# Kernel optimization log

Measured on AMD Instinct MI355X. Metric: run time of the kernel, lower is better.

## Reference

```python
import jax, jax.numpy as jnp
import numpy as np
from jax import lax

C = 768
CLS = 20
HEADS = 4
EPS = 1e-5


def setup_inputs() -> dict:
    key = jax.random.key(0)
    ks = jax.random.split(key, 16)
    B, Hp, Wp = 16, 32, 32
    s = 0.02
    return {
        "x_cls": jax.random.normal(ks[0], (B, CLS, C), jnp.float32),
        "input_patch": jax.random.normal(ks[1], (B, C, Hp, Wp), jnp.float32),
        # norm_cls (nn.LayerNorm)
        "ln_cls_w": jnp.ones((C,), jnp.float32),
        "ln_cls_b": jnp.zeros((C,), jnp.float32),
        # norm_x (LayerNormGeneral, affine_shape=(C,1,1))
        "nx_w": jnp.ones((C, 1, 1), jnp.float32),
        "nx_b": jnp.zeros((C, 1, 1), jnp.float32),
        # proj_q: Linear(C, C)
        "Wq": jax.random.normal(ks[2], (C, C), jnp.float32) * s,
        "bq": jnp.zeros((C,), jnp.float32),
        # proj_kv: Conv2d(C, 2C, 1)
        "Wkv": jax.random.normal(ks[3], (2 * C, C), jnp.float32) * s,
        "bkv": jnp.zeros((2 * C,), jnp.float32),
        # proj: Linear(C, C)
        "Wp": jax.random.normal(ks[4], (C, C), jnp.float32) * s,
        "bp": jnp.zeros((C,), jnp.float32),
        # proj_patch: Conv2d(CLS, C, 3, 1, 1) + BatchNorm2d(C) (eval) + GELU
        "Wconv": jax.random.normal(ks[5], (C, CLS, 3, 3), jnp.float32) * s,
        "bconv": jnp.zeros((C,), jnp.float32),
        "bn_g": jnp.ones((C,), jnp.float32),
        "bn_b": jnp.zeros((C,), jnp.float32),
        "bn_m": jnp.zeros((C,), jnp.float32),
        "bn_v": jnp.ones((C,), jnp.float32),
    }


def _layernorm_last(x, w, b):
    mu = x.mean(-1, keepdims=True)
    var = ((x - mu) ** 2).mean(-1, keepdims=True)
    return (x - mu) / jnp.sqrt(var + EPS) * w + b


def _layernorm_general(x, w, b):
    # normalized_dim=(1,2,3) on [B,C,H,W]; affine shape (C,1,1)
    mu = x.mean((1, 2, 3), keepdims=True)
    c = x - mu
    s = (c ** 2).mean((1, 2, 3), keepdims=True)
    return c / jnp.sqrt(s + EPS) * w + b


def reference(x_cls, input_patch, ln_cls_w, ln_cls_b, nx_w, nx_b, Wq, bq,
              Wkv, bkv, Wp, bp, Wconv, bconv, bn_g, bn_b, bn_m, bn_v):
    B, Cls, Cc = x_cls.shape
    Hp, Wpx = input_patch.shape[2:]
    dh = Cc // HEADS
    scale = dh ** (-0.5)

    # Q from cls tokens
    q = _layernorm_last(x_cls, ln_cls_w, ln_cls_b) @ Wq.T + bq  # [B,Cls,C]
    q = q.reshape(B, Cls, HEADS, dh).transpose(0, 2, 1, 3)      # [B,H,Cls,dh]

    # KV from conv patch features
    nx = _layernorm_general(input_patch, nx_w, nx_b)            # [B,C,Hp,Wp]
    kv = jnp.einsum('bchw,oc->bohw', nx, Wkv) + bkv[:, None, None]  # [B,2C,Hp,Wp]
    k, v = kv[:, :Cc], kv[:, Cc:]
    key = k.reshape(B, HEADS, dh, Hp * Wpx)                     # [B,H,dh,N]
    val = v.reshape(B, HEADS, dh, Hp * Wpx).transpose(0, 1, 3, 2)  # [B,H,N,dh]

    attn = jax.nn.softmax(jnp.einsum('bhcd,bhdn->bhcn', q, key) * scale, axis=-1)
    out = jnp.einsum('bhcn,bhnd->bhcd', attn, val)              # [B,H,Cls,dh]
    out = out.transpose(0, 2, 1, 3).reshape(B, Cls, Cc)
    out_cls = x_cls + (out @ Wp.T + bp)                         # proj_drop is identity (p=0)

    # semantic-to-feature projection
    patch_flat = input_patch.reshape(B, Cc, Hp * Wpx)           # [B,C,N]
    out_patch = jnp.einsum('blc,bcn->bln', out_cls, patch_flat) # [B,Cls,N]
    out_patch = out_patch.reshape(B, Cls, Hp, Wpx)

    y = lax.conv_general_dilated(out_patch, Wconv, (1, 1), 'SAME',
                                 dimension_numbers=('NCHW', 'OIHW', 'NCHW'))
    y = y + bconv[:, None, None]
    y = (y - bn_m[:, None, None]) / jnp.sqrt(bn_v[:, None, None] + EPS) \
        * bn_g[:, None, None] + bn_b[:, None, None]
    y = jax.nn.gelu(y, approximate=False)
    return out_cls, y
```

## Files before the change

kernel.cpp:

```cpp
#include <hip/hip_runtime.h>
#include <hip/hip_bf16.h>
#include <math.h>

typedef float f32x4 __attribute__((ext_vector_type(4)));
typedef __bf16 bf16x8 __attribute__((ext_vector_type(8)));
typedef __bf16 bf16x4 __attribute__((ext_vector_type(4)));


static constexpr size_t OFF_XT   = 0;
static constexpr size_t OFF_KT   = 25165824;
static constexpr size_t OFF_V    = 50331648;
static constexpr size_t OFF_WB   = 75497472;
static constexpr size_t OFF_RS   = 77856768;
static constexpr size_t OFF_CST  = 77862912;
static constexpr size_t OFF_PART = 77869056;
static constexpr size_t OFF_ST   = 77893632;
static constexpr size_t OFF_WQT  = 77893760;
static constexpr size_t OFF_WPT  = 80253056;
static constexpr size_t OFF_Q    = 82612352;
static constexpr size_t OFF_AO   = 83595392;
static constexpr size_t OFF_OP   = 84578432;

static constexpr size_t OFF_B2   = OFF_XT;
static constexpr size_t OFF_WCB  = OFF_XT + 6291456;
static constexpr size_t OFF_SC   = OFF_XT + 6586368;
static constexpr size_t OFF_SH   = OFF_XT + 6589440;

__global__ __launch_bounds__(256) void transpose_reduce(
    const float* __restrict__ x, __hip_bfloat16* __restrict__ xT,
    float* __restrict__ part) {
  __shared__ __hip_bfloat16 tile[64][66];
  __shared__ float red[4][2];
  int b = blockIdx.x, cb = blockIdx.y, nb = blockIdx.z;
  int t = threadIdx.x;
  const float* src = x + ((size_t)b * 768 + cb * 64) * 1024 + nb * 64;
  float s1 = 0.f, s2 = 0.f;
#pragma unroll
  for (int i = 0; i < 16; ++i) {
    int idx = i * 256 + t;
    int c = idx >> 6, n = idx & 63;
    float v = src[(size_t)c * 1024 + n];
    s1 += v; s2 += v * v;
    tile[c][n] = __float2bfloat16(v);
  }
#pragma unroll
  for (int o = 32; o > 0; o >>= 1) {
    s1 += __shfl_down(s1, o);
    s2 += __shfl_down(s2, o);
  }
  int wid = t >> 6, lane = t & 63;
  if (lane == 0) { red[wid][0] = s1; red[wid][1] = s2; }
  __syncthreads();
  if (t == 0) {
    float a = 0.f, bb = 0.f;
    for (int w = 0; w < 4; ++w) { a += red[w][0]; bb += red[w][1]; }
    int pidx = b * 192 + cb * 16 + nb;
    part[pidx * 2] = a; part[pidx * 2 + 1] = bb;
  }
  __hip_bfloat16* dst = xT + ((size_t)b * 1024 + nb * 64) * 768 + cb * 64;
#pragma unroll
  for (int i = 0; i < 16; ++i) {
    int idx = i * 256 + t;
    int n = idx >> 6, c = idx & 63;
    dst[(size_t)n * 768 + c] = tile[c][n];
  }
}

__global__ void finalize_stats(const float* __restrict__ part, float* __restrict__ st) {
  int t = threadIdx.x;
  if (t < 16) {
    float s1 = 0.f, s2 = 0.f;
    for (int i = 0; i < 192; ++i) {
      s1 += part[(t * 192 + i) * 2];
      s2 += part[(t * 192 + i) * 2 + 1];
    }
    float mu = s1 * (1.0f / 786432.0f);
    float var = s2 * (1.0f / 786432.0f) - mu * mu;
    st[t * 2] = mu;
    st[t * 2 + 1] = rsqrtf(var + 1e-5f);
  }
}

__global__ __launch_bounds__(256) void prep_wkv(
    const float* __restrict__ Wkv, const float* __restrict__ nxw,
    const float* __restrict__ nxb, const float* __restrict__ bkv,
    __hip_bfloat16* __restrict__ Wb, float* __restrict__ rowsum,
    float* __restrict__ cst) {
  int o = blockIdx.x * 4 + (threadIdx.x >> 6);
  int lane = threadIdx.x & 63;
  const float* wrow = Wkv + (size_t)o * 768;
  float rs = 0.f, cs = 0.f;
#pragma unroll
  for (int i = 0; i < 12; ++i) {
    int c = lane + i * 64;
    float w = wrow[c];
    float wb = w * nxw[c];
    Wb[(size_t)o * 768 + c] = __float2bfloat16(wb);
    rs += wb;
    cs += w * nxb[c];
  }
#pragma unroll
  for (int off = 32; off > 0; off >>= 1) {
    rs += __shfl_down(rs, off);
    cs += __shfl_down(cs, off);
  }
  if (lane == 0) { rowsum[o] = rs; cst[o] = cs + bkv[o]; }
}

__global__ __launch_bounds__(256) void transpose_w(
    const float* __restrict__ Wq, const float* __restrict__ Wp,
    float* __restrict__ WqT, float* __restrict__ WpT) {
  __shared__ float tl[64][65];
  const float* src = blockIdx.z ? Wp : Wq;
  float* dst = blockIdx.z ? WpT : WqT;
  int ot = blockIdx.x * 64, ct = blockIdx.y * 64;
  int t = threadIdx.x;
#pragma unroll
  for (int i = 0; i < 16; ++i) {
    int idx = i * 256 + t;
    int o = idx >> 6, c = idx & 63;
    tl[o][c] = src[(size_t)(ot + o) * 768 + ct + c];
  }
  __syncthreads();
#pragma unroll
  for (int i = 0; i < 16; ++i) {
    int idx = i * 256 + t;
    int c = idx >> 6, o = idx & 63;
    dst[(size_t)(ct + c) * 768 + ot + o] = tl[o][c];
  }
}

__global__ __launch_bounds__(256) void gemm_kv(
    const __hip_bfloat16* __restrict__ Wb, const __hip_bfloat16* __restrict__ xT,
    const float* __restrict__ rowsum, const float* __restrict__ cst,
    const float* __restrict__ st, __hip_bfloat16* __restrict__ KT,
    __hip_bfloat16* __restrict__ V) {
  __shared__ __hip_bfloat16 As[128 * 64];
  __shared__ __hip_bfloat16 Bs[128 * 64];
  int gx = blockIdx.x;
  int wg = (gx & 7) * 192 + (gx >> 3);
  int mt = wg % 12;
  int colt = wg / 12;
  int b = colt >> 3;
  int nt = colt & 7;
  int t = threadIdx.x;
  int wid = t >> 6, lane = t & 63;
  int wm = wid >> 1, wn = wid & 1;

  const __hip_bfloat16* Abase = Wb + (size_t)(mt * 128) * 768;
  const __hip_bfloat16* Bbase = xT + (size_t)b * 1024 * 768 + (size_t)(nt * 128) * 768;

  f32x4 acc[4][4] = {};

  for (int kt = 0; kt < 12; ++kt) {
    const __hip_bfloat16* ag = Abase + kt * 64;
    const __hip_bfloat16* bg = Bbase + kt * 64;
#pragma unroll
    for (int i = 0; i < 4; ++i) {
      int idx = i * 256 + t;
      int row = idx >> 3;
      int kc = (idx & 7) * 8;
      __builtin_amdgcn_global_load_lds(
          (const __attribute__((address_space(1))) void*)(ag + (size_t)row * 768 + kc),
          (__attribute__((address_space(3))) void*)(&As[idx * 8]), 16, 0, 0);
    }
#pragma unroll
    for (int i = 0; i < 4; ++i) {
      int idx = i * 256 + t;
      int row = idx >> 3;
      int kc = (idx & 7) * 8;
      __builtin_amdgcn_global_load_lds(
          (const __attribute__((address_space(1))) void*)(bg + (size_t)row * 768 + kc),
          (__attribute__((address_space(3))) void*)(&Bs[idx * 8]), 16, 0, 0);
    }
    __syncthreads();
#pragma unroll
    for (int kk = 0; kk < 2; ++kk) {
      bf16x8 af[4], bfv[4];
      int r = lane & 15, kc = kk * 32 + (lane >> 4) * 8;
#pragma unroll
      for (int mf = 0; mf < 4; ++mf)
        af[mf] = *(const bf16x8*)&As[(wm * 64 + mf * 16 + r) * 64 + kc];
#pragma unroll
      for (int nf = 0; nf < 4; ++nf)
        bfv[nf] = *(const bf16x8*)&Bs[(wn * 64 + nf * 16 + r) * 64 + kc];
#pragma unroll
      for (int mf = 0; mf < 4; ++mf)
#pragma unroll
        for (int nf = 0; nf < 4; ++nf)
          acc[mf][nf] = __builtin_amdgcn_mfma_f32_16x16x32_bf16(af[mf], bfv[nf], acc[mf][nf], 0, 0, 0);
    }
    __syncthreads();
  }
  float mu = st[b * 2], rstd = st[b * 2 + 1];
  if (mt < 6) {
    __hip_bfloat16* ktb = KT + (size_t)b * 1024 * 768;
#pragma unroll
    for (int mf = 0; mf < 4; ++mf) {
#pragma unroll
      for (int r = 0; r < 4; ++r) {
        int o = mt * 128 + wm * 64 + mf * 16 + (lane >> 4) * 4 + r;
        float corr = cst[o] - rstd * mu * rowsum[o];
#pragma unroll
        for (int nf = 0; nf < 4; ++nf) {
          int n = nt * 128 + wn * 64 + nf * 16 + (lane & 15);
          ktb[(size_t)n * 768 + o] = __float2bfloat16(rstd * acc[mf][nf][r] + corr);
        }
      }
    }
  } else {
    __hip_bfloat16* vb = V + (size_t)b * 768 * 1024;
#pragma unroll
    for (int mf = 0; mf < 4; ++mf) {
#pragma unroll
      for (int r = 0; r < 4; ++r) {
        int o = mt * 128 + wm * 64 + mf * 16 + (lane >> 4) * 4 + r;
        float corr = cst[o] - rstd * mu * rowsum[o];
        int ov = o - 768;
#pragma unroll
        for (int nf = 0; nf < 4; ++nf) {
          int n = nt * 128 + wn * 64 + nf * 16 + (lane & 15);
          vb[(size_t)ov * 1024 + n] = __float2bfloat16(rstd * acc[mf][nf][r] + corr);
        }
      }
    }
  }
}

__global__ __launch_bounds__(256) void q_proj(
    const float* __restrict__ x_cls, const float* __restrict__ lnw,
    const float* __restrict__ lnb, const float* __restrict__ WqT,
    const float* __restrict__ bq, __hip_bfloat16* __restrict__ Q) {
  __shared__ float xn[20 * 768];
  int b = blockIdx.x, ot = blockIdx.y;
  int t = threadIdx.x;
  const float* src = x_cls + (size_t)b * 20 * 768;
  for (int idx = t; idx < 15360; idx += 256) xn[idx] = src[idx];
  __syncthreads();
  int wid = t >> 6, lane = t & 63;
  for (int l = wid; l < 20; l += 4) {
    float s = 0.f;
#pragma unroll
    for (int i = 0; i < 12; ++i) s += xn[l * 768 + lane + i * 64];
#pragma unroll
    for (int o = 32; o > 0; o >>= 1) s += __shfl_down(s, o);
    s = __shfl(s, 0);
    float mu = s * (1.0f / 768.0f);
    float v = 0.f;
#pragma unroll
    for (int i = 0; i < 12; ++i) {
      float d = xn[l * 768 + lane + i * 64] - mu;
      v += d * d;
    }
#pragma unroll
    for (int o = 32; o > 0; o >>= 1) v += __shfl_down(v, o);
    v = __shfl(v, 0);
    float rstd = rsqrtf(v * (1.0f / 768.0f) + 1e-5f);
#pragma unroll
    for (int i = 0; i < 12; ++i) {
      int c = lane + i * 64;
      xn[l * 768 + c] = (xn[l * 768 + c] - mu) * rstd * lnw[c] + lnb[c];
    }
  }
  __syncthreads();
  int o = ot * 128 + (t & 127);
  int lg = t >> 7;
  float acc[10] = {};
  for (int c4 = 0; c4 < 768; c4 += 4) {
    float w0 = WqT[(size_t)(c4 + 0) * 768 + o];
    float w1 = WqT[(size_t)(c4 + 1) * 768 + o];
    float w2 = WqT[(size_t)(c4 + 2) * 768 + o];
    float w3 = WqT[(size_t)(c4 + 3) * 768 + o];
#pragma unroll
    for (int j = 0; j < 10; ++j) {
      const float4 a4 = *(const float4*)&xn[(lg * 10 + j) * 768 + c4];
      acc[j] += a4.x * w0 + a4.y * w1 + a4.z * w2 + a4.w * w3;
    }
  }
  float bqo = bq[o];
#pragma unroll
  for (int j = 0; j < 10; ++j)
    Q[((size_t)b * 20 + lg * 10 + j) * 768 + o] = __float2bfloat16(acc[j] + bqo);
}

__global__ __launch_bounds__(256) void attn_mfma(
    const __hip_bfloat16* __restrict__ Qbf, const __hip_bfloat16* __restrict__ KT,
    const __hip_bfloat16* __restrict__ V, float* __restrict__ AO) {
  __shared__ __hip_bfloat16 Qs[32 * 200];
  __shared__ __hip_bfloat16 Ps[32 * 1032];
  __shared__ float redm[4][32];
  __shared__ float reds[4][32];
  int b = blockIdx.x >> 2, h = blockIdx.x & 3;
  int t = threadIdx.x, w = t >> 6, lane = t & 63;
  int r16 = lane & 15, kg = lane >> 4;

  const __hip_bfloat16* qsrc = Qbf + (size_t)b * 20 * 768 + h * 192;
  for (int idx = t; idx < 32 * 192; idx += 256) {
    int l = idx / 192, d = idx % 192;
    Qs[l * 200 + d] = (l < 20) ? qsrc[(size_t)l * 768 + d] : __float2bfloat16(0.f);
  }
  __syncthreads();

  const __hip_bfloat16* ktb = KT + (size_t)b * 1024 * 768 + h * 192;
  int n0 = w * 256;
  f32x4 acc[2][16] = {};
  for (int ks = 0; ks < 6; ++ks) {
    bf16x8 af0 = *(const bf16x8*)&Qs[(r16) * 200 + ks * 32 + kg * 8];
    bf16x8 af1 = *(const bf16x8*)&Qs[(16 + r16) * 200 + ks * 32 + kg * 8];
#pragma unroll
    for (int nt = 0; nt < 16; ++nt) {
      bf16x8 bfv = *(const bf16x8*)&ktb[(size_t)(n0 + nt * 16 + r16) * 768 + ks * 32 + kg * 8];
      acc[0][nt] = __builtin_amdgcn_mfma_f32_16x16x32_bf16(af0, bfv, acc[0][nt], 0, 0, 0);
      acc[1][nt] = __builtin_amdgcn_mfma_f32_16x16x32_bf16(af1, bfv, acc[1][nt], 0, 0, 0);
    }
  }

#pragma unroll
  for (int mf = 0; mf < 2; ++mf) {
#pragma unroll
    for (int r = 0; r < 4; ++r) {
      float m = acc[mf][0][r];
#pragma unroll
      for (int nt = 1; nt < 16; ++nt) m = fmaxf(m, acc[mf][nt][r]);
#pragma unroll
      for (int o = 1; o < 16; o <<= 1) m = fmaxf(m, __shfl_xor(m, o));
      if (r16 == 0) redm[w][mf * 16 + kg * 4 + r] = m;
    }
  }
  __syncthreads();

  const float scale = 0.07216878364870322f;
#pragma unroll
  for (int mf = 0; mf < 2; ++mf) {
#pragma unroll
    for (int r = 0; r < 4; ++r) {
      int row = mf * 16 + kg * 4 + r;
      float M = fmaxf(fmaxf(redm[0][row], redm[1][row]),
                      fmaxf(redm[2][row], redm[3][row]));
      float s = 0.f;
#pragma unroll
      for (int nt = 0; nt < 16; ++nt) {
        float e = __expf((acc[mf][nt][r] - M) * scale);
        s += e;
        Ps[row * 1032 + n0 + nt * 16 + r16] = __float2bfloat16(e);
      }
#pragma unroll
      for (int o = 1; o < 16; o <<= 1) s += __shfl_xor(s, o);
      if (r16 == 0) reds[w][row] = s;
    }
  }
  __syncthreads();

  const __hip_bfloat16* vb = V + ((size_t)b * 768 + h * 192 + w * 48) * 1024;
  f32x4 pacc[2][3] = {};
  for (int ks = 0; ks < 32; ++ks) {
    bf16x8 pa0 = *(const bf16x8*)&Ps[(r16) * 1032 + ks * 32 + kg * 8];
    bf16x8 pa1 = *(const bf16x8*)&Ps[(16 + r16) * 1032 + ks * 32 + kg * 8];
#pragma unroll
    for (int nt = 0; nt < 3; ++nt) {
      bf16x8 vf = *(const bf16x8*)&vb[(size_t)(nt * 16 + r16) * 1024 + ks * 32 + kg * 8];
      pacc[0][nt] = __builtin_amdgcn_mfma_f32_16x16x32_bf16(pa0, vf, pacc[0][nt], 0, 0, 0);
      pacc[1][nt] = __builtin_amdgcn_mfma_f32_16x16x32_bf16(pa1, vf, pacc[1][nt], 0, 0, 0);
    }
  }

#pragma unroll
  for (int mf = 0; mf < 2; ++mf) {
#pragma unroll
    for (int r = 0; r < 4; ++r) {
      int row = mf * 16 + kg * 4 + r;
      if (row < 20) {
        float rinv = 1.0f / (reds[0][row] + reds[1][row] + reds[2][row] + reds[3][row]);
#pragma unroll
        for (int nt = 0; nt < 3; ++nt) {
          int d = w * 48 + nt * 16 + r16;
          AO[((size_t)b * 20 + row) * 768 + h * 192 + d] = pacc[mf][nt][r] * rinv;
        }
      }
    }
  }
}

__global__ __launch_bounds__(256) void cls_proj(
    const float* __restrict__ AO, const float* __restrict__ x_cls,
    const float* __restrict__ WpT, const float* __restrict__ bp,
    float* __restrict__ out_cls) {
  __shared__ float a[20 * 768];
  int b = blockIdx.x, ot = blockIdx.y;
  int t = threadIdx.x;
  const float* src = AO + (size_t)b * 15360;
  for (int idx = t; idx < 15360; idx += 256) a[idx] = src[idx];
  __syncthreads();
  int o = ot * 128 + (t & 127);
  int lg = t >> 7;
  float acc[10] = {};
  for (int c4 = 0; c4 < 768; c4 += 4) {
    float w0 = WpT[(size_t)(c4 + 0) * 768 + o];
    float w1 = WpT[(size_t)(c4 + 1) * 768 + o];
    float w2 = WpT[(size_t)(c4 + 2) * 768 + o];
    float w3 = WpT[(size_t)(c4 + 3) * 768 + o];
#pragma unroll
    for (int j = 0; j < 10; ++j) {
      const float4 a4 = *(const float4*)&a[(lg * 10 + j) * 768 + c4];
      acc[j] += a4.x * w0 + a4.y * w1 + a4.z * w2 + a4.w * w3;
    }
  }
  float bpo = bp[o];
#pragma unroll
  for (int j = 0; j < 10; ++j) {
    int l = lg * 10 + j;
    out_cls[((size_t)b * 20 + l) * 768 + o] =
        x_cls[((size_t)b * 20 + l) * 768 + o] + acc[j] + bpo;
  }
}

__global__ __launch_bounds__(256) void patch_mm(
    const float* __restrict__ out_cls, const float* __restrict__ x,
    float* __restrict__ OP) {
  __shared__ float a[20 * 768];
  int b = blockIdx.x, nt2 = blockIdx.y;
  int t = threadIdx.x;
  const float* src = out_cls + (size_t)b * 15360;
  for (int idx = t; idx < 15360; idx += 256) a[idx] = src[idx];
  __syncthreads();
  int n = nt2 * 128 + (t & 127);
  int lg = t >> 7;
  const float* xb = x + (size_t)b * 768 * 1024 + n;
  float acc[10] = {};
  for (int c4 = 0; c4 < 768; c4 += 4) {
    float x0 = xb[(size_t)(c4 + 0) * 1024];
    float x1 = xb[(size_t)(c4 + 1) * 1024];
    float x2 = xb[(size_t)(c4 + 2) * 1024];
    float x3 = xb[(size_t)(c4 + 3) * 1024];
#pragma unroll
    for (int j = 0; j < 10; ++j) {
      const float4 a4 = *(const float4*)&a[(lg * 10 + j) * 768 + c4];
      acc[j] += a4.x * x0 + a4.y * x1 + a4.z * x2 + a4.w * x3;
    }
  }
#pragma unroll
  for (int j = 0; j < 10; ++j)
    OP[((size_t)b * 20 + lg * 10 + j) * 1024 + n] = acc[j];
}

__global__ __launch_bounds__(192) void prep_wconv(
    const float* __restrict__ Wc, const float* __restrict__ bc,
    const float* __restrict__ bng, const float* __restrict__ bnb,
    const float* __restrict__ bnm, const float* __restrict__ bnv,
    __hip_bfloat16* __restrict__ Wcb, float* __restrict__ sc,
    float* __restrict__ sh) {
  int oc = blockIdx.x;
  int k = threadIdx.x;
  float v = (k < 180) ? Wc[(size_t)oc * 180 + k] : 0.0f;
  Wcb[(size_t)oc * 192 + k] = __float2bfloat16(v);
  if (k == 0) {
    float s = bng[oc] * rsqrtf(bnv[oc] + 1e-5f);
    sc[oc] = s;
    sh[oc] = (bc[oc] - bnm[oc]) * s + bnb[oc];
  }
}

__global__ __launch_bounds__(256) void im2col(
    const float* __restrict__ OP, __hip_bfloat16* __restrict__ Bm) {
  int idx = blockIdx.x * 256 + threadIdx.x;
  int b = idx / (1024 * 96);
  int r = idx % (1024 * 96);
  int n = r / 96;
  int kp = (r % 96) * 2;
  int y = n >> 5, x = n & 31;
  const float* pb = OP + (size_t)b * 20 * 1024;
  float v[2];
#pragma unroll
  for (int j = 0; j < 2; ++j) {
    int k = kp + j;
    float val = 0.0f;
    if (k < 180) {
      int ic = k / 9, k9 = k % 9;
      int kh = k9 / 3, kw = k9 % 3;
      int yy = y + kh - 1, xx = x + kw - 1;
      if (yy >= 0 && yy < 32 && xx >= 0 && xx < 32)
        val = pb[ic * 1024 + yy * 32 + xx];
    }
    v[j] = val;
  }
  __hip_bfloat162 o2;
  o2.x = __float2bfloat16(v[0]);
  o2.y = __float2bfloat16(v[1]);
  *(__hip_bfloat162*)&Bm[(size_t)idx * 2] = o2;
}

__global__ __launch_bounds__(256) void gemm_conv(
    const __hip_bfloat16* __restrict__ Wcb, const __hip_bfloat16* __restrict__ Bm,
    const float* __restrict__ sc, const float* __restrict__ sh,
    float* __restrict__ y) {
  __shared__ __hip_bfloat16 As[128 * 64];
  __shared__ __hip_bfloat16 Bs[128 * 64];
  int gx = blockIdx.x;
  int wg = (gx & 7) * 96 + (gx >> 3);
  int mt = wg % 6;
  int colt = wg / 6;
  int b = colt >> 3;
  int nt = colt & 7;
  int t = threadIdx.x;
  int wid = t >> 6, lane = t & 63;
  int wm = wid >> 1, wn = wid & 1;

  const __hip_bfloat16* Abase = Wcb + (size_t)(mt * 128) * 192;
  const __hip_bfloat16* Bbase = Bm + ((size_t)b * 1024 + nt * 128) * 192;

  f32x4 acc[4][4] = {};

  for (int kt = 0; kt < 3; ++kt) {
    const __hip_bfloat16* ag = Abase + kt * 64;
    const __hip_bfloat16* bg = Bbase + kt * 64;
#pragma unroll
    for (int i = 0; i < 4; ++i) {
      int idx = i * 256 + t;
      int row = idx >> 3;
      int kc = (idx & 7) * 8;
      __builtin_amdgcn_global_load_lds(
          (const __attribute__((address_space(1))) void*)(ag + (size_t)row * 192 + kc),
          (__attribute__((address_space(3))) void*)(&As[idx * 8]), 16, 0, 0);
    }
#pragma unroll
    for (int i = 0; i < 4; ++i) {
      int idx = i * 256 + t;
      int row = idx >> 3;
      int kc = (idx & 7) * 8;
      __builtin_amdgcn_global_load_lds(
          (const __attribute__((address_space(1))) void*)(bg + (size_t)row * 192 + kc),
          (__attribute__((address_space(3))) void*)(&Bs[idx * 8]), 16, 0, 0);
    }
    __syncthreads();
#pragma unroll
    for (int kk = 0; kk < 2; ++kk) {
      bf16x8 af[4], bfv[4];
      int r = lane & 15, kc = kk * 32 + (lane >> 4) * 8;
#pragma unroll
      for (int mf = 0; mf < 4; ++mf)
        af[mf] = *(const bf16x8*)&As[(wm * 64 + mf * 16 + r) * 64 + kc];
#pragma unroll
      for (int nf = 0; nf < 4; ++nf)
        bfv[nf] = *(const bf16x8*)&Bs[(wn * 64 + nf * 16 + r) * 64 + kc];
#pragma unroll
      for (int mf = 0; mf < 4; ++mf)
#pragma unroll
        for (int nf = 0; nf < 4; ++nf)
          acc[mf][nf] = __builtin_amdgcn_mfma_f32_16x16x32_bf16(af[mf], bfv[nf], acc[mf][nf], 0, 0, 0);
    }
    __syncthreads();
  }
  float* yb = y + (size_t)b * 768 * 1024;
#pragma unroll
  for (int mf = 0; mf < 4; ++mf) {
#pragma unroll
    for (int r = 0; r < 4; ++r) {
      int oc = mt * 128 + wm * 64 + mf * 16 + (lane >> 4) * 4 + r;
      float s = sc[oc], h = sh[oc];
#pragma unroll
      for (int nf = 0; nf < 4; ++nf) {
        int n = nt * 128 + wn * 64 + nf * 16 + (lane & 15);
        float val = acc[mf][nf][r] * s + h;
        yb[(size_t)oc * 1024 + n] = 0.5f * val * (1.0f + erff(val * 0.70710678118f));
      }
    }
  }
}

extern "C" void kernel_launch(void* const* d_in, const int* in_sizes, int n_in,
                              void* d_out, int out_size, void* d_ws, size_t ws_size,
                              hipStream_t stream) {
  (void)in_sizes; (void)n_in; (void)out_size; (void)ws_size;
  const float* x_cls = (const float*)d_in[0];
  const float* x     = (const float*)d_in[1];
  const float* lnw   = (const float*)d_in[2];
  const float* lnb   = (const float*)d_in[3];
  const float* nxw   = (const float*)d_in[4];
  const float* nxb   = (const float*)d_in[5];
  const float* Wq    = (const float*)d_in[6];
  const float* bq    = (const float*)d_in[7];
  const float* Wkv   = (const float*)d_in[8];
  const float* bkv   = (const float*)d_in[9];
  const float* Wp    = (const float*)d_in[10];
  const float* bp    = (const float*)d_in[11];
  const float* Wc    = (const float*)d_in[12];
  const float* bc    = (const float*)d_in[13];
  const float* bng   = (const float*)d_in[14];
  const float* bnb   = (const float*)d_in[15];
  const float* bnm   = (const float*)d_in[16];
  const float* bnv   = (const float*)d_in[17];

  char* w = (char*)d_ws;
  __hip_bfloat16* xT = (__hip_bfloat16*)(w + OFF_XT);
  __hip_bfloat16* KT = (__hip_bfloat16*)(w + OFF_KT);
  __hip_bfloat16* V  = (__hip_bfloat16*)(w + OFF_V);
  __hip_bfloat16* Wb = (__hip_bfloat16*)(w + OFF_WB);
  float* rs   = (float*)(w + OFF_RS);
  float* cst  = (float*)(w + OFF_CST);
  float* part = (float*)(w + OFF_PART);
  float* st   = (float*)(w + OFF_ST);
  float* WqT  = (float*)(w + OFF_WQT);
  float* WpT  = (float*)(w + OFF_WPT);
  __hip_bfloat16* Qb = (__hip_bfloat16*)(w + OFF_Q);
  float* AO   = (float*)(w + OFF_AO);
  float* OP   = (float*)(w + OFF_OP);
  __hip_bfloat16* Bm  = (__hip_bfloat16*)(w + OFF_B2);
  __hip_bfloat16* Wcb = (__hip_bfloat16*)(w + OFF_WCB);
  float* scb  = (float*)(w + OFF_SC);
  float* shb  = (float*)(w + OFF_SH);

  float* out_cls = (float*)d_out;
  float* y = out_cls + 245760;

  transpose_reduce<<<dim3(16, 12, 16), 256, 0, stream>>>(x, xT, part);
  finalize_stats<<<1, 64, 0, stream>>>(part, st);
  prep_wkv<<<384, 256, 0, stream>>>(Wkv, nxw, nxb, bkv, Wb, rs, cst);
  transpose_w<<<dim3(12, 12, 2), 256, 0, stream>>>(Wq, Wp, WqT, WpT);
  gemm_kv<<<1536, 256, 0, stream>>>(Wb, xT, rs, cst, st, KT, V);
  prep_wconv<<<768, 192, 0, stream>>>(Wc, bc, bng, bnb, bnm, bnv, Wcb, scb, shb);
  q_proj<<<dim3(16, 6), 256, 0, stream>>>(x_cls, lnw, lnb, WqT, bq, Qb);
  attn_mfma<<<64, 256, 0, stream>>>(Qb, KT, V, AO);
  cls_proj<<<dim3(16, 6), 256, 0, stream>>>(AO, x_cls, WpT, bp, out_cls);
  patch_mm<<<dim3(16, 8), 256, 0, stream>>>(out_cls, x, OP);
  im2col<<<6144, 256, 0, stream>>>(OP, Bm);
  gemm_conv<<<768, 256, 0, stream>>>(Wcb, Bm, scb, shb, y);
}
```

Baseline: 456.8 us.

## Double-buffer LDS in KV and conv GEMMs, split attention PV across 8 waves

The KV-projection and conv GEMMs now use two LDS buffers, so the global-to-LDS load of the next K tile is issued before the MFMAs on the current tile, overlapping memory latency with compute. The attention kernel grows from 256 to 512 threads. Each wave handles half as many keys for QK/softmax, and the PV product is split over two key halves whose partial sums are combined through shared memory. LDS use doubles in the GEMMs, which may lower occupancy, and the attention kernel gains an extra barrier and a reduction step.

```diff
diff --git a/kernel.cpp b/kernel.cpp
--- a/kernel.cpp
+++ b/kernel.cpp
@@ -130,13 +130,56 @@
   }
 }
 
+
+#define STAGE_KV(buf, kt) do {                                                  \
+  const __hip_bfloat16* ag_ = Abase + (kt) * 64;                                \
+  const __hip_bfloat16* bg_ = Bbase + (kt) * 64;                                \
+  _Pragma("unroll")                                                             \
+  for (int i_ = 0; i_ < 4; ++i_) {                                              \
+    int idx_ = i_ * 256 + t;                                                    \
+    int row_ = idx_ >> 3;                                                       \
+    int kc_ = (idx_ & 7) * 8;                                                   \
+    __builtin_amdgcn_global_load_lds(                                           \
+        (const __attribute__((address_space(1))) void*)(ag_ + (size_t)row_ * 768 + kc_), \
+        (__attribute__((address_space(3))) void*)(&As[buf][idx_ * 8]), 16, 0, 0); \
+  }                                                                             \
+  _Pragma("unroll")                                                             \
+  for (int i_ = 0; i_ < 4; ++i_) {                                              \
+    int idx_ = i_ * 256 + t;                                                    \
+    int row_ = idx_ >> 3;                                                       \
+    int kc_ = (idx_ & 7) * 8;                                                   \
+    __builtin_amdgcn_global_load_lds(                                           \
+        (const __attribute__((address_space(1))) void*)(bg_ + (size_t)row_ * 768 + kc_), \
+        (__attribute__((address_space(3))) void*)(&Bs[buf][idx_ * 8]), 16, 0, 0); \
+  }                                                                             \
+} while (0)
+
+#define COMPUTE_KV(buf) do {                                                    \
+  _Pragma("unroll")                                                             \
+  for (int kk_ = 0; kk_ < 2; ++kk_) {                                           \
+    bf16x8 af_[4], bfv_[4];                                                     \
+    int r_ = lane & 15, kc_ = kk_ * 32 + (lane >> 4) * 8;                       \
+    _Pragma("unroll")                                                           \
+    for (int mf_ = 0; mf_ < 4; ++mf_)                                           \
+      af_[mf_] = *(const bf16x8*)&As[buf][(wm * 64 + mf_ * 16 + r_) * 64 + kc_]; \
+    _Pragma("unroll")                                                           \
+    for (int nf_ = 0; nf_ < 4; ++nf_)                                           \
+      bfv_[nf_] = *(const bf16x8*)&Bs[buf][(wn * 64 + nf_ * 16 + r_) * 64 + kc_]; \
+    _Pragma("unroll")                                                           \
+    for (int mf_ = 0; mf_ < 4; ++mf_)                                           \
+      _Pragma("unroll")                                                         \
+      for (int nf_ = 0; nf_ < 4; ++nf_)                                         \
+        acc[mf_][nf_] = __builtin_amdgcn_mfma_f32_16x16x32_bf16(af_[mf_], bfv_[nf_], acc[mf_][nf_], 0, 0, 0); \
+  }                                                                             \
+} while (0)
+
 __global__ __launch_bounds__(256) void gemm_kv(
     const __hip_bfloat16* __restrict__ Wb, const __hip_bfloat16* __restrict__ xT,
     const float* __restrict__ rowsum, const float* __restrict__ cst,
     const float* __restrict__ st, __hip_bfloat16* __restrict__ KT,
     __hip_bfloat16* __restrict__ V) {
-  __shared__ __hip_bfloat16 As[128 * 64];
-  __shared__ __hip_bfloat16 Bs[128 * 64];
+  __shared__ __hip_bfloat16 As[2][128 * 64];
+  __shared__ __hip_bfloat16 Bs[2][128 * 64];
   int gx = blockIdx.x;
   int wg = (gx & 7) * 192 + (gx >> 3);
   int mt = wg % 12;
@@ -152,46 +195,18 @@
 
   f32x4 acc[4][4] = {};
 
-  for (int kt = 0; kt < 12; ++kt) {
-    const __hip_bfloat16* ag = Abase + kt * 64;
-    const __hip_bfloat16* bg = Bbase + kt * 64;
-#pragma unroll
-    for (int i = 0; i < 4; ++i) {
-      int idx = i * 256 + t;
-      int row = idx >> 3;
-      int kc = (idx & 7) * 8;
-      __builtin_amdgcn_global_load_lds(
-          (const __attribute__((address_space(1))) void*)(ag + (size_t)row * 768 + kc),
-          (__attribute__((address_space(3))) void*)(&As[idx * 8]), 16, 0, 0);
-    }
-#pragma unroll
-    for (int i = 0; i < 4; ++i) {
-      int idx = i * 256 + t;
-      int row = idx >> 3;
-      int kc = (idx & 7) * 8;
-      __builtin_amdgcn_global_load_lds(
-          (const __attribute__((address_space(1))) void*)(bg + (size_t)row * 768 + kc),
-          (__attribute__((address_space(3))) void*)(&Bs[idx * 8]), 16, 0, 0);
-    }
+  STAGE_KV(0, 0);
+  __syncthreads();
+#pragma unroll 1
+  for (int kt2 = 0; kt2 < 6; ++kt2) {
+    STAGE_KV(1, 2 * kt2 + 1);
+    COMPUTE_KV(0);
     __syncthreads();
-#pragma unroll
-    for (int kk = 0; kk < 2; ++kk) {
-      bf16x8 af[4], bfv[4];
-      int r = lane & 15, kc = kk * 32 + (lane >> 4) * 8;
-#pragma unroll
-      for (int mf = 0; mf < 4; ++mf)
-        af[mf] = *(const bf16x8*)&As[(wm * 64 + mf * 16 + r) * 64 + kc];
-#pragma unroll
-      for (int nf = 0; nf < 4; ++nf)
-        bfv[nf] = *(const bf16x8*)&Bs[(wn * 64 + nf * 16 + r) * 64 + kc];
-#pragma unroll
-      for (int mf = 0; mf < 4; ++mf)
-#pragma unroll
-        for (int nf = 0; nf < 4; ++nf)
-          acc[mf][nf] = __builtin_amdgcn_mfma_f32_16x16x32_bf16(af[mf], bfv[nf], acc[mf][nf], 0, 0, 0);
-    }
+    if (kt2 < 5) STAGE_KV(0, 2 * kt2 + 2);
+    COMPUTE_KV(1);
     __syncthreads();
   }
+
   float mu = st[b * 2], rstd = st[b * 2 + 1];
   if (mt < 6) {
     __hip_bfloat16* ktb = KT + (size_t)b * 1024 * 768;
@@ -283,32 +298,33 @@
     Q[((size_t)b * 20 + lg * 10 + j) * 768 + o] = __float2bfloat16(acc[j] + bqo);
 }
 
-__global__ __launch_bounds__(256) void attn_mfma(
+__global__ __launch_bounds__(512) void attn_mfma(
     const __hip_bfloat16* __restrict__ Qbf, const __hip_bfloat16* __restrict__ KT,
     const __hip_bfloat16* __restrict__ V, float* __restrict__ AO) {
   __shared__ __hip_bfloat16 Qs[32 * 200];
   __shared__ __hip_bfloat16 Ps[32 * 1032];
-  __shared__ float redm[4][32];
-  __shared__ float reds[4][32];
+  __shared__ float redm[8][32];
+  __shared__ float reds[8][32];
+  __shared__ float pvp[4][32][48];
   int b = blockIdx.x >> 2, h = blockIdx.x & 3;
   int t = threadIdx.x, w = t >> 6, lane = t & 63;
   int r16 = lane & 15, kg = lane >> 4;
 
   const __hip_bfloat16* qsrc = Qbf + (size_t)b * 20 * 768 + h * 192;
-  for (int idx = t; idx < 32 * 192; idx += 256) {
+  for (int idx = t; idx < 32 * 192; idx += 512) {
     int l = idx / 192, d = idx % 192;
     Qs[l * 200 + d] = (l < 20) ? qsrc[(size_t)l * 768 + d] : __float2bfloat16(0.f);
   }
   __syncthreads();
 
   const __hip_bfloat16* ktb = KT + (size_t)b * 1024 * 768 + h * 192;
-  int n0 = w * 256;
-  f32x4 acc[2][16] = {};
+  int n0 = w * 128;
+  f32x4 acc[2][8] = {};
   for (int ks = 0; ks < 6; ++ks) {
     bf16x8 af0 = *(const bf16x8*)&Qs[(r16) * 200 + ks * 32 + kg * 8];
     bf16x8 af1 = *(const bf16x8*)&Qs[(16 + r16) * 200 + ks * 32 + kg * 8];
 #pragma unroll
-    for (int nt = 0; nt < 16; ++nt) {
+    for (int nt = 0; nt < 8; ++nt) {
       bf16x8 bfv = *(const bf16x8*)&ktb[(size_t)(n0 + nt * 16 + r16) * 768 + ks * 32 + kg * 8];
       acc[0][nt] = __builtin_amdgcn_mfma_f32_16x16x32_bf16(af0, bfv, acc[0][nt], 0, 0, 0);
       acc[1][nt] = __builtin_amdgcn_mfma_f32_16x16x32_bf16(af1, bfv, acc[1][nt], 0, 0, 0);
@@ -321,7 +337,7 @@
     for (int r = 0; r < 4; ++r) {
       float m = acc[mf][0][r];
 #pragma unroll
-      for (int nt = 1; nt < 16; ++nt) m = fmaxf(m, acc[mf][nt][r]);
+      for (int nt = 1; nt < 8; ++nt) m = fmaxf(m, acc[mf][nt][r]);
 #pragma unroll
       for (int o = 1; o < 16; o <<= 1) m = fmaxf(m, __shfl_xor(m, o));
       if (r16 == 0) redm[w][mf * 16 + kg * 4 + r] = m;
@@ -335,11 +351,13 @@
 #pragma unroll
     for (int r = 0; r < 4; ++r) {
       int row = mf * 16 + kg * 4 + r;
-      float M = fmaxf(fmaxf(redm[0][row], redm[1][row]),
-                      fmaxf(redm[2][row], redm[3][row]));
+      float M = fmaxf(fmaxf(fmaxf(redm[0][row], redm[1][row]),
+                            fmaxf(redm[2][row], redm[3][row])),
+                      fmaxf(fmaxf(redm[4][row], redm[5][row]),
+                            fmaxf(redm[6][row], redm[7][row])));
       float s = 0.f;
 #pragma unroll
-      for (int nt = 0; nt < 16; ++nt) {
+      for (int nt = 0; nt < 8; ++nt) {
         float e = __expf((acc[mf][nt][r] - M) * scale);
         s += e;
         Ps[row * 1032 + n0 + nt * 16 + r16] = __float2bfloat16(e);
@@ -351,9 +369,10 @@
   }
   __syncthreads();
 
-  const __hip_bfloat16* vb = V + ((size_t)b * 768 + h * 192 + w * 48) * 1024;
+  int wd = w & 3, kh = w >> 2;
+  const __hip_bfloat16* vb = V + ((size_t)b * 768 + h * 192 + wd * 48) * 1024;
   f32x4 pacc[2][3] = {};
-  for (int ks = 0; ks < 32; ++ks) {
+  for (int ks = kh * 16; ks < kh * 16 + 16; ++ks) {
     bf16x8 pa0 = *(const bf16x8*)&Ps[(r16) * 1032 + ks * 32 + kg * 8];
     bf16x8 pa1 = *(const bf16x8*)&Ps[(16 + r16) * 1032 + ks * 32 + kg * 8];
 #pragma unroll
@@ -363,18 +382,33 @@
       pacc[1][nt] = __builtin_amdgcn_mfma_f32_16x16x32_bf16(pa1, vf, pacc[1][nt], 0, 0, 0);
     }
   }
-
-#pragma unroll
-  for (int mf = 0; mf < 2; ++mf) {
-#pragma unroll
-    for (int r = 0; r < 4; ++r) {
-      int row = mf * 16 + kg * 4 + r;
-      if (row < 20) {
-        float rinv = 1.0f / (reds[0][row] + reds[1][row] + reds[2][row] + reds[3][row]);
-#pragma unroll
-        for (int nt = 0; nt < 3; ++nt) {
-          int d = w * 48 + nt * 16 + r16;
-          AO[((size_t)b * 20 + row) * 768 + h * 192 + d] = pacc[mf][nt][r] * rinv;
+  if (w >= 4) {
+#pragma unroll
+    for (int mf = 0; mf < 2; ++mf)
+#pragma unroll
+      for (int r = 0; r < 4; ++r)
+#pragma unroll
+        for (int nt = 0; nt < 3; ++nt)
+          pvp[wd][mf * 16 + kg * 4 + r][nt * 16 + r16] = pacc[mf][nt][r];
+  }
+  __syncthreads();
+
+  if (w < 4) {
+#pragma unroll
+    for (int mf = 0; mf < 2; ++mf) {
+#pragma unroll
+      for (int r = 0; r < 4; ++r) {
+        int row = mf * 16 + kg * 4 + r;
+        if (row < 20) {
+          float rs8 = reds[0][row] + reds[1][row] + reds[2][row] + reds[3][row] +
+                      reds[4][row] + reds[5][row] + reds[6][row] + reds[7][row];
+          float rinv = 1.0f / rs8;
+#pragma unroll
+          for (int nt = 0; nt < 3; ++nt) {
+            int d = wd * 48 + nt * 16 + r16;
+            AO[((size_t)b * 20 + row) * 768 + h * 192 + d] =
+                (pacc[mf][nt][r] + pvp[wd][row][nt * 16 + r16]) * rinv;
+          }
         }
       }
     }
@@ -489,12 +523,36 @@
   *(__hip_bfloat162*)&Bm[(size_t)idx * 2] = o2;
 }
 
+
+#define STAGE_CV(buf, kt) do {                                                  \
+  const __hip_bfloat16* ag_ = Abase + (kt) * 64;                                \
+  const __hip_bfloat16* bg_ = Bbase + (kt) * 64;                                \
+  _Pragma("unroll")                                                             \
+  for (int i_ = 0; i_ < 4; ++i_) {                                              \
+    int idx_ = i_ * 256 + t;                                                    \
+    int row_ = idx_ >> 3;                                                       \
+    int kc_ = (idx_ & 7) * 8;                                                   \
+    __builtin_amdgcn_global_load_lds(                                           \
+        (const __attribute__((address_space(1))) void*)(ag_ + (size_t)row_ * 192 + kc_), \
+        (__attribute__((address_space(3))) void*)(&As[buf][idx_ * 8]), 16, 0, 0); \
+  }                                                                             \
+  _Pragma("unroll")                                                             \
+  for (int i_ = 0; i_ < 4; ++i_) {                                              \
+    int idx_ = i_ * 256 + t;                                                    \
+    int row_ = idx_ >> 3;                                                       \
+    int kc_ = (idx_ & 7) * 8;                                                   \
+    __builtin_amdgcn_global_load_lds(                                           \
+        (const __attribute__((address_space(1))) void*)(bg_ + (size_t)row_ * 192 + kc_), \
+        (__attribute__((address_space(3))) void*)(&Bs[buf][idx_ * 8]), 16, 0, 0); \
+  }                                                                             \
+} while (0)
+
 __global__ __launch_bounds__(256) void gemm_conv(
     const __hip_bfloat16* __restrict__ Wcb, const __hip_bfloat16* __restrict__ Bm,
     const float* __restrict__ sc, const float* __restrict__ sh,
     float* __restrict__ y) {
-  __shared__ __hip_bfloat16 As[128 * 64];
-  __shared__ __hip_bfloat16 Bs[128 * 64];
+  __shared__ __hip_bfloat16 As[2][128 * 64];
+  __shared__ __hip_bfloat16 Bs[2][128 * 64];
   int gx = blockIdx.x;
   int wg = (gx & 7) * 96 + (gx >> 3);
   int mt = wg % 6;
@@ -510,46 +568,16 @@
 
   f32x4 acc[4][4] = {};
 
-  for (int kt = 0; kt < 3; ++kt) {
-    const __hip_bfloat16* ag = Abase + kt * 64;
-    const __hip_bfloat16* bg = Bbase + kt * 64;
-#pragma unroll
-    for (int i = 0; i < 4; ++i) {
-      int idx = i * 256 + t;
-      int row = idx >> 3;
-      int kc = (idx & 7) * 8;
-      __builtin_amdgcn_global_load_lds(
-          (const __attribute__((address_space(1))) void*)(ag + (size_t)row * 192 + kc),
-          (__attribute__((address_space(3))) void*)(&As[idx * 8]), 16, 0, 0);
-    }
-#pragma unroll
-    for (int i = 0; i < 4; ++i) {
-      int idx = i * 256 + t;
-      int row = idx >> 3;
-      int kc = (idx & 7) * 8;
-      __builtin_amdgcn_global_load_lds(
-          (const __attribute__((address_space(1))) void*)(bg + (size_t)row * 192 + kc),
-          (__attribute__((address_space(3))) void*)(&Bs[idx * 8]), 16, 0, 0);
-    }
-    __syncthreads();
-#pragma unroll
-    for (int kk = 0; kk < 2; ++kk) {
-      bf16x8 af[4], bfv[4];
-      int r = lane & 15, kc = kk * 32 + (lane >> 4) * 8;
-#pragma unroll
-      for (int mf = 0; mf < 4; ++mf)
-        af[mf] = *(const bf16x8*)&As[(wm * 64 + mf * 16 + r) * 64 + kc];
-#pragma unroll
-      for (int nf = 0; nf < 4; ++nf)
-        bfv[nf] = *(const bf16x8*)&Bs[(wn * 64 + nf * 16 + r) * 64 + kc];
-#pragma unroll
-      for (int mf = 0; mf < 4; ++mf)
-#pragma unroll
-        for (int nf = 0; nf < 4; ++nf)
-          acc[mf][nf] = __builtin_amdgcn_mfma_f32_16x16x32_bf16(af[mf], bfv[nf], acc[mf][nf], 0, 0, 0);
-    }
-    __syncthreads();
-  }
+  STAGE_CV(0, 0);
+  __syncthreads();
+  STAGE_CV(1, 1);
+  COMPUTE_KV(0);
+  __syncthreads();
+  STAGE_CV(0, 2);
+  COMPUTE_KV(1);
+  __syncthreads();
+  COMPUTE_KV(0);
+
   float* yb = y + (size_t)b * 768 * 1024;
 #pragma unroll
   for (int mf = 0; mf < 4; ++mf) {
@@ -619,7 +647,7 @@
   gemm_kv<<<1536, 256, 0, stream>>>(Wb, xT, rs, cst, st, KT, V);
   prep_wconv<<<768, 192, 0, stream>>>(Wc, bc, bng, bnb, bnm, bnv, Wcb, scb, shb);
   q_proj<<<dim3(16, 6), 256, 0, stream>>>(x_cls, lnw, lnb, WqT, bq, Qb);
-  attn_mfma<<<64, 256, 0, stream>>>(Qb, KT, V, AO);
+  attn_mfma<<<64, 512, 0, stream>>>(Qb, KT, V, AO);
   cls_proj<<<dim3(16, 6), 256, 0, stream>>>(AO, x_cls, WpT, bp, out_cls);
   patch_mm<<<dim3(16, 8), 256, 0, stream>>>(out_cls, x, OP);
   im2col<<<6144, 256, 0, stream>>>(OP, Bm);
```

New measurement: 449.8 us. Within noise of the previous version (-1.5%).
